# Kernel tuning notes

Measured on AMD Instinct MI355X. Metric: run time of the kernel, lower is better.

## Reference

```python
import jax, jax.numpy as jnp
import numpy as np

ALPHA = 0.2          # LeakyReLU negative slope
NEG = -9e15          # mask fill value, as in pyGAT GraphAttentionLayer
N, NIN, NHID, NOUT = 4096, 64, 32, 64
NHEADS, D_INT = 8, 32
H_INT = max(1, int(NHEADS * 0.25))   # 2 intent heads
H_SP = NHEADS - H_INT                # 6 spatial heads


def setup_inputs() -> dict:
    key = jax.random.key(0)
    ks = jax.random.split(key, 10)
    x = jax.random.normal(ks[0], (N, NIN), dtype=jnp.float32)
    adj = (jax.random.uniform(ks[1], (N, N)) < 0.01).astype(jnp.float32)
    adj = jnp.clip(adj + jnp.eye(N, dtype=jnp.float32), 0.0, 1.0)
    intent_embeds = jax.random.normal(ks[2], (N, D_INT), dtype=jnp.float32)
    # learned params (xavier-ish scale)
    def xav(k, shape):
        fan = shape[-2] if len(shape) > 1 else shape[-1]
        return jax.random.normal(k, shape, dtype=jnp.float32) / np.sqrt(fan)
    W_sp = xav(ks[3], (H_SP, NIN, NHID))       # spatial head projections
    a_sp = xav(ks[4], (H_SP, 2 * NHID))        # spatial attention vectors
    W_int = xav(ks[5], (H_INT, NIN, NHID))     # intent head projections
    a_int = xav(ks[6], (H_INT, 2 * D_INT))     # intent attention vectors (over intent embeds)
    W_out = xav(ks[7], (NHID * NHEADS, NOUT))  # output GAT layer
    a_out = xav(ks[8], (2 * NOUT,))
    return {"x": x, "adj": adj, "intent_embeds": intent_embeds,
            "W_sp": W_sp, "a_sp": a_sp, "W_int": W_int, "a_int": a_int,
            "W_out": W_out, "a_out": a_out}


def _masked_attend(e, mask, Wh):
    # e: [H,N,N] raw scores, mask: [1,N,N] bool, Wh: [H,N,F]
    att = jax.nn.softmax(jnp.where(mask, e, NEG), axis=-1)
    return jnp.einsum('hij,hjf->hif', att, Wh)


def reference(x, adj, intent_embeds, W_sp, a_sp, W_int, a_int, W_out, a_out):
    mask = (adj > 0)[None]                                   # [1,N,N]
    # ---- spatial heads (standard GAT, batched over heads) ----
    Wh_s = jnp.einsum('nf,hfo->hno', x, W_sp)                # [Hs,N,nhid]
    f1 = jnp.einsum('hno,ho->hn', Wh_s, a_sp[:, :NHID])
    f2 = jnp.einsum('hno,ho->hn', Wh_s, a_sp[:, NHID:])
    e_s = jax.nn.leaky_relu(f1[:, :, None] + f2[:, None, :], ALPHA)
    h_s = jax.nn.elu(_masked_attend(e_s, mask, Wh_s))        # concat=True -> elu
    # ---- intent heads: scores from intent embeddings, values from Wh ----
    Wh_i = jnp.einsum('nf,hfo->hno', x, W_int)               # [Hi,N,nhid]
    g1 = jnp.einsum('nd,hd->hn', intent_embeds, a_int[:, :D_INT])
    g2 = jnp.einsum('nd,hd->hn', intent_embeds, a_int[:, D_INT:])
    e_i = jax.nn.leaky_relu(g1[:, :, None] + g2[:, None, :], ALPHA)
    h_i = jax.nn.elu(_masked_attend(e_i, mask, Wh_i))        # [Hi,N,nhid]
    # ---- concat heads along feature dim: [N, nheads*nhid] ----
    h = jnp.concatenate([h_s, h_i], axis=0).transpose(1, 0, 2).reshape(N, -1)
    # ---- output attention layer (concat=False: no elu) ----
    Who = h @ W_out                                          # [N,nout]
    o1 = Who @ a_out[:NOUT]
    o2 = Who @ a_out[NOUT:]
    e_o = jax.nn.leaky_relu(o1[:, None] + o2[None, :], ALPHA)
    att_o = jax.nn.softmax(jnp.where(mask[0], e_o, NEG), axis=-1)
    out = att_o @ Who
    return jnp.tanh(out)
```

## Files before the change

kernel.cpp:

```cpp
#include <hip/hip_runtime.h>

#define N      4096
#define NIN    64
#define NHID   32
#define NOUT   64
#define NHEADS 8
#define H_SP   6
#define D_INT  32
#define MAXDEG 128
#define ALPHA  0.2f

__global__ __launch_bounds__(256) void k_csr(
    const float4* __restrict__ adj4, int* __restrict__ col, int* __restrict__ deg)
{
    const int wave = threadIdx.x >> 6;
    const int lane = threadIdx.x & 63;
    const int r = blockIdx.x * 4 + wave;
    const float4* row = adj4 + (size_t)r * (N / 4);

    int cnt = 0;
#pragma unroll 4
    for (int base = 0; base < N / 4; base += 64) {
        float4 v = row[base + lane];
        unsigned nib = (v.x > 0.f ? 1u : 0u) | (v.y > 0.f ? 2u : 0u)
                     | (v.z > 0.f ? 4u : 0u) | (v.w > 0.f ? 8u : 0u);
        int c = __popc(nib);
        int scan = c;
#pragma unroll
        for (int m = 1; m <= 32; m <<= 1) {
            int o = __shfl_up(scan, m);
            if (lane >= m) scan += o;
        }
        int pos = cnt + scan - c;
        int total = __shfl(scan, 63);
        int idx0 = (base + lane) * 4;
        if (nib) {
            if (nib & 1u) { if (pos < MAXDEG) col[r * MAXDEG + pos] = idx0;     ++pos; }
            if (nib & 2u) { if (pos < MAXDEG) col[r * MAXDEG + pos] = idx0 + 1; ++pos; }
            if (nib & 4u) { if (pos < MAXDEG) col[r * MAXDEG + pos] = idx0 + 2; ++pos; }
            if (nib & 8u) { if (pos < MAXDEG) col[r * MAXDEG + pos] = idx0 + 3; ++pos; }
        }
        cnt += total;
    }
    if (lane == 0) deg[r] = (cnt < MAXDEG) ? cnt : MAXDEG;
}

__global__ __launch_bounds__(256) void k_proj(
    const float* __restrict__ x, const float* __restrict__ ie,
    const float* __restrict__ Wsp, const float* __restrict__ asp,
    const float* __restrict__ Wint, const float* __restrict__ aint,
    float* __restrict__ Wh, float* __restrict__ src, float* __restrict__ dst)
{
    const int n = blockIdx.x;
    const int tid = threadIdx.x;
    const int h = tid >> 5, f = tid & 31;

    __shared__ float xs[NIN];
    __shared__ float ies[D_INT];
    if (tid < NIN) xs[tid] = x[n * NIN + tid];
    else if (tid < NIN + D_INT) ies[tid - NIN] = ie[n * D_INT + (tid - NIN)];
    __syncthreads();

    const float* W = (h < H_SP) ? (Wsp + h * NIN * NHID)
                                : (Wint + (h - H_SP) * NIN * NHID);
    float acc = 0.f;
#pragma unroll
    for (int c = 0; c < NIN; ++c) acc += xs[c] * W[c * NHID + f];
    Wh[((size_t)h * N + n) * NHID + f] = acc;

    float s1, s2;
    if (h < H_SP) {
        s1 = acc * asp[h * 2 * NHID + f];
        s2 = acc * asp[h * 2 * NHID + NHID + f];
    } else {
        float v = ies[f];
        s1 = v * aint[(h - H_SP) * 2 * D_INT + f];
        s2 = v * aint[(h - H_SP) * 2 * D_INT + D_INT + f];
    }
#pragma unroll
    for (int m = 16; m >= 1; m >>= 1) {
        s1 += __shfl_xor(s1, m);
        s2 += __shfl_xor(s2, m);
    }
    if (f == 0) { src[h * N + n] = s1; dst[h * N + n] = s2; }
}

__global__ __launch_bounds__(256) void k_attn1who(
    const int* __restrict__ col, const int* __restrict__ deg,
    const float* __restrict__ Wh, const float* __restrict__ src,
    const float* __restrict__ dst, const float* __restrict__ Wout,
    const float* __restrict__ aout,
    float* __restrict__ Who, float* __restrict__ o1, float* __restrict__ o2)
{
    const int r = blockIdx.x;
    const int tid = threadIdx.x;
    const int h = tid >> 5, lane = tid & 31;

    __shared__ int cs[MAXDEG];
    __shared__ float w[NHEADS][MAXDEG];
    __shared__ float hs[NHEADS * NHID];
    __shared__ float part[4][NOUT];

    const int d = deg[r];
    for (int k = tid; k < d; k += 256) cs[k] = col[r * MAXDEG + k];
    __syncthreads();

    const float sr = src[h * N + r];
    const float* dsth = dst + h * N;

    float ev[4];
    float mx = -3.4e38f;
#pragma unroll
    for (int t = 0; t < 4; ++t) {
        int k = lane + t * 32;
        float e = -3.4e38f;
        if (k < d) {
            e = sr + dsth[cs[k]];
            e = e > 0.f ? e : ALPHA * e;
        }
        ev[t] = e;
        mx = fmaxf(mx, e);
    }
#pragma unroll
    for (int m = 16; m >= 1; m >>= 1) mx = fmaxf(mx, __shfl_xor(mx, m));

    float sum = 0.f;
#pragma unroll
    for (int t = 0; t < 4; ++t) {
        int k = lane + t * 32;
        float p = (k < d) ? __expf(ev[t] - mx) : 0.f;
        ev[t] = p;
        sum += p;
    }
#pragma unroll
    for (int m = 16; m >= 1; m >>= 1) sum += __shfl_xor(sum, m);
    const float inv = 1.f / sum;

#pragma unroll
    for (int t = 0; t < 4; ++t) {
        int k = lane + t * 32;
        if (k < d) w[h][k] = ev[t] * inv;
    }
    __syncthreads();

    const float* Whh = Wh + (size_t)h * N * NHID;
    float acc = 0.f;
    for (int k = 0; k < d; ++k) acc += w[h][k] * Whh[(size_t)cs[k] * NHID + lane];
    acc = acc > 0.f ? acc : __expf(acc) - 1.f;
    hs[h * NHID + lane] = acc;
    __syncthreads();

    const int f = tid & 63, q = tid >> 6;
    float p = 0.f;
#pragma unroll
    for (int c = q * 64; c < q * 64 + 64; ++c) p += hs[c] * Wout[c * NOUT + f];
    part[q][f] = p;
    __syncthreads();

    if (tid < 64) {
        float who = part[0][tid] + part[1][tid] + part[2][tid] + part[3][tid];
        Who[(size_t)r * NOUT + tid] = who;
        float v1 = who * aout[tid];
        float v2 = who * aout[NOUT + tid];
#pragma unroll
        for (int m = 32; m >= 1; m >>= 1) {
            v1 += __shfl_xor(v1, m);
            v2 += __shfl_xor(v2, m);
        }
        if (tid == 0) { o1[r] = v1; o2[r] = v2; }
    }
}

__global__ __launch_bounds__(64) void k_attn2(
    const int* __restrict__ col, const int* __restrict__ deg,
    const float* __restrict__ Who, const float* __restrict__ o1,
    const float* __restrict__ o2, float* __restrict__ out)
{
    const int r = blockIdx.x, lane = threadIdx.x;
    __shared__ int cs[MAXDEG];
    __shared__ float w[MAXDEG];

    const int d = deg[r];
    for (int k = lane; k < d; k += 64) cs[k] = col[r * MAXDEG + k];
    __syncthreads();

    const float sr = o1[r];
    float ev[2];
    float mx = -3.4e38f;
#pragma unroll
    for (int t = 0; t < 2; ++t) {
        int k = lane + t * 64;
        float e = -3.4e38f;
        if (k < d) {
            e = sr + o2[cs[k]];
            e = e > 0.f ? e : ALPHA * e;
        }
        ev[t] = e;
        mx = fmaxf(mx, e);
    }
#pragma unroll
    for (int m = 32; m >= 1; m >>= 1) mx = fmaxf(mx, __shfl_xor(mx, m));

    float sum = 0.f;
#pragma unroll
    for (int t = 0; t < 2; ++t) {
        int k = lane + t * 64;
        float p = (k < d) ? __expf(ev[t] - mx) : 0.f;
        ev[t] = p;
        sum += p;
    }
#pragma unroll
    for (int m = 32; m >= 1; m >>= 1) sum += __shfl_xor(sum, m);
    const float inv = 1.f / sum;
#pragma unroll
    for (int t = 0; t < 2; ++t) {
        int k = lane + t * 64;
        if (k < d) w[k] = ev[t] * inv;
    }
    __syncthreads();

    float acc = 0.f;
    for (int k = 0; k < d; ++k) acc += w[k] * Who[(size_t)cs[k] * NOUT + lane];
    out[(size_t)r * NOUT + lane] = tanhf(acc);
}

extern "C" void kernel_launch(void* const* d_in, const int* in_sizes, int n_in,
                              void* d_out, int out_size, void* d_ws, size_t ws_size,
                              hipStream_t stream) {
    const float* x    = (const float*)d_in[0];
    const float* adj  = (const float*)d_in[1];
    const float* ie   = (const float*)d_in[2];
    const float* Wsp  = (const float*)d_in[3];
    const float* asp  = (const float*)d_in[4];
    const float* Wint = (const float*)d_in[5];
    const float* aint = (const float*)d_in[6];
    const float* Wout = (const float*)d_in[7];
    const float* aout = (const float*)d_in[8];
    float* out = (float*)d_out;

    float* ws   = (float*)d_ws;
    float* Wh   = ws;
    float* src  = Wh   + 1048576;
    float* dst  = src  + 32768;
    float* Who  = dst  + 32768;
    float* o1   = Who  + 262144;
    float* o2   = o1   + 4096;
    int*   col  = (int*)(o2 + 4096);
    int*   deg  = col + 4096 * MAXDEG;

    k_csr     <<<N / 4, 256, 0, stream>>>((const float4*)adj, col, deg);
    k_proj    <<<N,     256, 0, stream>>>(x, ie, Wsp, asp, Wint, aint, Wh, src, dst);
    k_attn1who<<<N,     256, 0, stream>>>(col, deg, Wh, src, dst, Wout, aout, Who, o1, o2);
    k_attn2   <<<N,      64, 0, stream>>>(col, deg, Who, o1, o2, out);
}
```

Before: 164.9 us.

## Fuse CSR build into projection kernel, node-major Wh layout, widen attn2

```diff
diff --git a/kernel.cpp b/kernel.cpp
--- a/kernel.cpp
+++ b/kernel.cpp
@@ -8,55 +8,33 @@
 #define H_SP   6
 #define D_INT  32
 #define MAXDEG 128
+#define WCAP   80
 #define ALPHA  0.2f
 
-__global__ __launch_bounds__(256) void k_csr(
-    const float4* __restrict__ adj4, int* __restrict__ col, int* __restrict__ deg)
-{
-    const int wave = threadIdx.x >> 6;
-    const int lane = threadIdx.x & 63;
-    const int r = blockIdx.x * 4 + wave;
-    const float4* row = adj4 + (size_t)r * (N / 4);
-
-    int cnt = 0;
-#pragma unroll 4
-    for (int base = 0; base < N / 4; base += 64) {
-        float4 v = row[base + lane];
-        unsigned nib = (v.x > 0.f ? 1u : 0u) | (v.y > 0.f ? 2u : 0u)
-                     | (v.z > 0.f ? 4u : 0u) | (v.w > 0.f ? 8u : 0u);
-        int c = __popc(nib);
-        int scan = c;
-#pragma unroll
-        for (int m = 1; m <= 32; m <<= 1) {
-            int o = __shfl_up(scan, m);
-            if (lane >= m) scan += o;
-        }
-        int pos = cnt + scan - c;
-        int total = __shfl(scan, 63);
-        int idx0 = (base + lane) * 4;
-        if (nib) {
-            if (nib & 1u) { if (pos < MAXDEG) col[r * MAXDEG + pos] = idx0;     ++pos; }
-            if (nib & 2u) { if (pos < MAXDEG) col[r * MAXDEG + pos] = idx0 + 1; ++pos; }
-            if (nib & 4u) { if (pos < MAXDEG) col[r * MAXDEG + pos] = idx0 + 2; ++pos; }
-            if (nib & 8u) { if (pos < MAXDEG) col[r * MAXDEG + pos] = idx0 + 3; ++pos; }
-        }
-        cnt += total;
-    }
-    if (lane == 0) deg[r] = (cnt < MAXDEG) ? cnt : MAXDEG;
-}
-
-__global__ __launch_bounds__(256) void k_proj(
+__global__ __launch_bounds__(256) void k_fused1(
     const float* __restrict__ x, const float* __restrict__ ie,
+    const float4* __restrict__ adj4,
     const float* __restrict__ Wsp, const float* __restrict__ asp,
     const float* __restrict__ Wint, const float* __restrict__ aint,
-    float* __restrict__ Wh, float* __restrict__ src, float* __restrict__ dst)
+    float* __restrict__ Wh_t, float* __restrict__ src, float* __restrict__ dst_t,
+    int* __restrict__ col, int* __restrict__ deg)
 {
-    const int n = blockIdx.x;
-    const int tid = threadIdx.x;
-    const int h = tid >> 5, f = tid & 31;
+    const int n    = blockIdx.x;
+    const int tid  = threadIdx.x;
+    const int wv   = tid >> 6, lane = tid & 63;
+    const int h    = tid >> 5, f    = tid & 31;
 
     __shared__ float xs[NIN];
     __shared__ float ies[D_INT];
+    __shared__ int   wbuf[4][WCAP];
+    __shared__ int   wcnt[4];
+
+    const float4* row = adj4 + (size_t)n * (N / 4) + wv * 256 + lane;
+    float4 a0 = row[0];
+    float4 a1 = row[64];
+    float4 a2 = row[128];
+    float4 a3 = row[192];
+
     if (tid < NIN) xs[tid] = x[n * NIN + tid];
     else if (tid < NIN + D_INT) ies[tid - NIN] = ie[n * D_INT + (tid - NIN)];
     __syncthreads();
@@ -66,7 +44,7 @@
     float acc = 0.f;
 #pragma unroll
     for (int c = 0; c < NIN; ++c) acc += xs[c] * W[c * NHID + f];
-    Wh[((size_t)h * N + n) * NHID + f] = acc;
+    Wh_t[(size_t)n * 256 + tid] = acc;
 
     float s1, s2;
     if (h < H_SP) {
@@ -82,32 +60,70 @@
         s1 += __shfl_xor(s1, m);
         s2 += __shfl_xor(s2, m);
     }
-    if (f == 0) { src[h * N + n] = s1; dst[h * N + n] = s2; }
+    if (f == 0) { src[h * N + n] = s1; dst_t[n * 8 + h] = s2; }
+
+    int cnt = 0;
+#pragma unroll
+    for (int t = 0; t < 4; ++t) {
+        float4 v = (t == 0) ? a0 : (t == 1) ? a1 : (t == 2) ? a2 : a3;
+        unsigned nib = (v.x > 0.f ? 1u : 0u) | (v.y > 0.f ? 2u : 0u)
+                     | (v.z > 0.f ? 4u : 0u) | (v.w > 0.f ? 8u : 0u);
+        int c = __popc(nib);
+        int scan = c;
+#pragma unroll
+        for (int m = 1; m <= 32; m <<= 1) {
+            int o = __shfl_up(scan, m);
+            if (lane >= m) scan += o;
+        }
+        int pos = cnt + scan - c;
+        int idx0 = (wv * 256 + t * 64 + lane) * 4;
+        if (nib) {
+            if (nib & 1u) { if (pos < WCAP) wbuf[wv][pos] = idx0;     ++pos; }
+            if (nib & 2u) { if (pos < WCAP) wbuf[wv][pos] = idx0 + 1; ++pos; }
+            if (nib & 4u) { if (pos < WCAP) wbuf[wv][pos] = idx0 + 2; ++pos; }
+            if (nib & 8u) { if (pos < WCAP) wbuf[wv][pos] = idx0 + 3; ++pos; }
+        }
+        cnt += __shfl(scan, 63);
+    }
+    if (lane == 0) wcnt[wv] = cnt;
+    __syncthreads();
+
+    const int c0 = wcnt[0], c1 = wcnt[1], c2 = wcnt[2], c3 = wcnt[3];
+    const int off = (wv > 0 ? c0 : 0) + (wv > 1 ? c1 : 0) + (wv > 2 ? c2 : 0);
+    const int my = (wcnt[wv] < WCAP) ? wcnt[wv] : WCAP;
+    for (int i = lane; i < my; i += 64) {
+        int p = off + i;
+        if (p < MAXDEG) col[n * MAXDEG + p] = wbuf[wv][i];
+    }
+    if (tid == 0) {
+        int tot = c0 + c1 + c2 + c3;
+        deg[n] = (tot < MAXDEG) ? tot : MAXDEG;
+    }
 }
 
 __global__ __launch_bounds__(256) void k_attn1who(
     const int* __restrict__ col, const int* __restrict__ deg,
-    const float* __restrict__ Wh, const float* __restrict__ src,
-    const float* __restrict__ dst, const float* __restrict__ Wout,
+    const float* __restrict__ Wh_t, const float* __restrict__ src,
+    const float* __restrict__ dst_t, const float* __restrict__ Wout,
     const float* __restrict__ aout,
     float* __restrict__ Who, float* __restrict__ o1, float* __restrict__ o2)
 {
-    const int r = blockIdx.x;
+    const int r   = blockIdx.x;
     const int tid = threadIdx.x;
-    const int h = tid >> 5, lane = tid & 31;
-
-    __shared__ int cs[MAXDEG];
+    const int h   = tid >> 5, lane = tid & 31;
+
+    __shared__ int   cs[MAXDEG];
     __shared__ float w[NHEADS][MAXDEG];
     __shared__ float hs[NHEADS * NHID];
     __shared__ float part[4][NOUT];
 
-    const int d = deg[r];
-    for (int k = tid; k < d; k += 256) cs[k] = col[r * MAXDEG + k];
+    const int d  = deg[r];
+    const int d4 = (d + 3) & ~3;
+    for (int k = tid; k < MAXDEG; k += 256)
+        cs[k] = (k < d) ? col[r * MAXDEG + k] : 0;
     __syncthreads();
 
     const float sr = src[h * N + r];
-    const float* dsth = dst + h * N;
-
     float ev[4];
     float mx = -3.4e38f;
 #pragma unroll
@@ -115,7 +131,7 @@
         int k = lane + t * 32;
         float e = -3.4e38f;
         if (k < d) {
-            e = sr + dsth[cs[k]];
+            e = sr + dst_t[cs[k] * 8 + h];
             e = e > 0.f ? e : ALPHA * e;
         }
         ev[t] = e;
@@ -139,22 +155,29 @@
 #pragma unroll
     for (int t = 0; t < 4; ++t) {
         int k = lane + t * 32;
-        if (k < d) w[h][k] = ev[t] * inv;
-    }
-    __syncthreads();
-
-    const float* Whh = Wh + (size_t)h * N * NHID;
+        w[h][k] = (k < d) ? ev[t] * inv : 0.f;
+    }
+    __syncthreads();
+
     float acc = 0.f;
-    for (int k = 0; k < d; ++k) acc += w[h][k] * Whh[(size_t)cs[k] * NHID + lane];
+    for (int k = 0; k < d4; k += 4) {
+        int4   j4 = *(const int4*)  &cs[k];
+        float4 w4 = *(const float4*)&w[h][k];
+        float g0 = Wh_t[(size_t)j4.x * 256 + tid];
+        float g1 = Wh_t[(size_t)j4.y * 256 + tid];
+        float g2 = Wh_t[(size_t)j4.z * 256 + tid];
+        float g3 = Wh_t[(size_t)j4.w * 256 + tid];
+        acc += w4.x * g0 + w4.y * g1 + w4.z * g2 + w4.w * g3;
+    }
     acc = acc > 0.f ? acc : __expf(acc) - 1.f;
-    hs[h * NHID + lane] = acc;
-    __syncthreads();
-
-    const int f = tid & 63, q = tid >> 6;
+    hs[tid] = acc;
+    __syncthreads();
+
+    const int fo = tid & 63, q = tid >> 6;
     float p = 0.f;
 #pragma unroll
-    for (int c = q * 64; c < q * 64 + 64; ++c) p += hs[c] * Wout[c * NOUT + f];
-    part[q][f] = p;
+    for (int c = q * 64; c < q * 64 + 64; ++c) p += hs[c] * Wout[c * NOUT + fo];
+    part[q][fo] = p;
     __syncthreads();
 
     if (tid < 64) {
@@ -171,57 +194,64 @@
     }
 }
 
-__global__ __launch_bounds__(64) void k_attn2(
+__global__ __launch_bounds__(256) void k_attn2(
     const int* __restrict__ col, const int* __restrict__ deg,
     const float* __restrict__ Who, const float* __restrict__ o1,
     const float* __restrict__ o2, float* __restrict__ out)
 {
-    const int r = blockIdx.x, lane = threadIdx.x;
-    __shared__ int cs[MAXDEG];
+    const int r   = blockIdx.x;
+    const int tid = threadIdx.x;
+    const int wv  = tid >> 6, lane = tid & 63;
+
+    __shared__ int   cs[MAXDEG];
     __shared__ float w[MAXDEG];
-
-    const int d = deg[r];
-    for (int k = lane; k < d; k += 64) cs[k] = col[r * MAXDEG + k];
+    __shared__ float part[4][NOUT];
+    __shared__ float redm[4], reds[4];
+
+    const int d  = deg[r];
+    const int d4 = (d + 3) & ~3;
+    for (int k = tid; k < MAXDEG; k += 256)
+        cs[k] = (k < d) ? col[r * MAXDEG + k] : 0;
     __syncthreads();
 
     const float sr = o1[r];
-    float ev[2];
-    float mx = -3.4e38f;
-#pragma unroll
-    for (int t = 0; t < 2; ++t) {
-        int k = lane + t * 64;
-        float e = -3.4e38f;
-        if (k < d) {
-            e = sr + o2[cs[k]];
-            e = e > 0.f ? e : ALPHA * e;
-        }
-        ev[t] = e;
-        mx = fmaxf(mx, e);
-    }
+    float e = -3.4e38f;
+    if (tid < d) {
+        e = sr + o2[cs[tid]];
+        e = e > 0.f ? e : ALPHA * e;
+    }
+    float mx = e;
 #pragma unroll
     for (int m = 32; m >= 1; m >>= 1) mx = fmaxf(mx, __shfl_xor(mx, m));
-
-    float sum = 0.f;
-#pragma unroll
-    for (int t = 0; t < 2; ++t) {
-        int k = lane + t * 64;
-        float p = (k < d) ? __expf(ev[t] - mx) : 0.f;
-        ev[t] = p;
-        sum += p;
-    }
-#pragma unroll
-    for (int m = 32; m >= 1; m >>= 1) sum += __shfl_xor(sum, m);
-    const float inv = 1.f / sum;
-#pragma unroll
-    for (int t = 0; t < 2; ++t) {
-        int k = lane + t * 64;
-        if (k < d) w[k] = ev[t] * inv;
-    }
+    if (lane == 0) redm[wv] = mx;
+    __syncthreads();
+    mx = fmaxf(fmaxf(redm[0], redm[1]), fmaxf(redm[2], redm[3]));
+
+    float p = (tid < d) ? __expf(e - mx) : 0.f;
+    float s = p;
+#pragma unroll
+    for (int m = 32; m >= 1; m >>= 1) s += __shfl_xor(s, m);
+    if (lane == 0) reds[wv] = s;
+    __syncthreads();
+    const float inv = 1.f / (reds[0] + reds[1] + reds[2] + reds[3]);
+    if (tid < MAXDEG) w[tid] = p * inv;
     __syncthreads();
 
     float acc = 0.f;
-    for (int k = 0; k < d; ++k) acc += w[k] * Who[(size_t)cs[k] * NOUT + lane];
-    out[(size_t)r * NOUT + lane] = tanhf(acc);
+    for (int k = wv * 4; k < d4; k += 16) {
+        int4   j4 = *(const int4*)  &cs[k];
+        float4 w4 = *(const float4*)&w[k];
+        acc += w4.x * Who[(size_t)j4.x * NOUT + lane];
+        acc += w4.y * Who[(size_t)j4.y * NOUT + lane];
+        acc += w4.z * Who[(size_t)j4.z * NOUT + lane];
+        acc += w4.w * Who[(size_t)j4.w * NOUT + lane];
+    }
+    part[wv][lane] = acc;
+    __syncthreads();
+
+    if (tid < NOUT)
+        out[(size_t)r * NOUT + tid] =
+            tanhf(part[0][tid] + part[1][tid] + part[2][tid] + part[3][tid]);
 }
 
 extern "C" void kernel_launch(void* const* d_in, const int* in_sizes, int n_in,
@@ -238,18 +268,19 @@
     const float* aout = (const float*)d_in[8];
     float* out = (float*)d_out;
 
-    float* ws   = (float*)d_ws;
-    float* Wh   = ws;
-    float* src  = Wh   + 1048576;
-    float* dst  = src  + 32768;
-    float* Who  = dst  + 32768;
-    float* o1   = Who  + 262144;
-    float* o2   = o1   + 4096;
-    int*   col  = (int*)(o2 + 4096);
-    int*   deg  = col + 4096 * MAXDEG;
-
-    k_csr     <<<N / 4, 256, 0, stream>>>((const float4*)adj, col, deg);
-    k_proj    <<<N,     256, 0, stream>>>(x, ie, Wsp, asp, Wint, aint, Wh, src, dst);
-    k_attn1who<<<N,     256, 0, stream>>>(col, deg, Wh, src, dst, Wout, aout, Who, o1, o2);
-    k_attn2   <<<N,      64, 0, stream>>>(col, deg, Who, o1, o2, out);
-}
+    float* ws    = (float*)d_ws;
+    float* Wh_t  = ws;
+    float* src   = Wh_t + 1048576;
+    float* dst_t = src  + 32768;
+    float* Who   = dst_t + 32768;
+    float* o1    = Who  + 262144;
+    float* o2    = o1   + 4096;
+    int*   col   = (int*)(o2 + 4096);
+    int*   deg   = col + 4096 * MAXDEG;
+
+    k_fused1  <<<N, 256, 0, stream>>>(x, ie, (const float4*)adj, Wsp, asp,
+                                      Wint, aint, Wh_t, src, dst_t, col, deg);
+    k_attn1who<<<N, 256, 0, stream>>>(col, deg, Wh_t, src, dst_t, Wout, aout,
+                                      Who, o1, o2);
+    k_attn2   <<<N, 256, 0, stream>>>(col, deg, Who, o1, o2, out);
+}
```

Result: faster. 158.0 us (-4.2%).
